# Performance work log

Measured on AMD Instinct MI355X. Metric: run time of the kernel, lower is better.

The kernel has to match this reference:

```python
import jax, jax.numpy as jnp
import numpy as np

H = 128          # rnn_hid_size
SEQ_LEN = 2048
B = 4096
IN = 2           # SELECT_SIZE * 2


def _uniform(key, shape, stdv):
    return jax.random.uniform(key, shape, jnp.float32, -stdv, stdv)


def setup_inputs() -> dict:
    key = jax.random.key(0)
    ks = jax.random.split(key, 20)
    values = jax.random.normal(ks[0], (B, SEQ_LEN, 3), jnp.float32)
    masks = (jax.random.uniform(ks[1], (B, SEQ_LEN)) > 0.5).astype(jnp.float32)
    deltas = jax.random.uniform(ks[2], (B, SEQ_LEN, 3), jnp.float32)
    eval_masks = (jax.random.uniform(ks[3], (B, SEQ_LEN)) > 0.5).astype(jnp.float32)
    s = 1.0 / np.sqrt(H)
    params = {
        'Wih0': _uniform(ks[4], (4 * H, IN), s), 'Whh0': _uniform(ks[5], (4 * H, H), s),
        'bih0': _uniform(ks[6], (4 * H,), s), 'bhh0': _uniform(ks[7], (4 * H,), s),
        'Wih1': _uniform(ks[8], (4 * H, IN), s), 'Whh1': _uniform(ks[9], (4 * H, H), s),
        'bih1': _uniform(ks[10], (4 * H,), s), 'bhh1': _uniform(ks[11], (4 * H,), s),
        'td_W': _uniform(ks[12], (H, 1), s), 'td_b': _uniform(ks[13], (H,), s),
        'hr_W': _uniform(ks[14], (1, H), 1.0 / np.sqrt(H)), 'hr_b': _uniform(ks[15], (1,), 1.0 / np.sqrt(H)),
    }
    return dict(values=values, masks=masks, deltas=deltas, eval_masks=eval_masks, **params)


def _lstm_cell(x, h, c, Wih, Whh, bih, bhh):
    g = x @ Wih.T + bih + h @ Whh.T + bhh            # [B, 4H]
    i, f, gg, o = jnp.split(g, 4, axis=1)
    c2 = jax.nn.sigmoid(f) * c + jax.nn.sigmoid(i) * jnp.tanh(gg)
    h2 = jax.nn.sigmoid(o) * jnp.tanh(c2)
    return h2, c2


def reference(values, masks, deltas, eval_masks,
              Wih0, Whh0, bih0, bhh0, Wih1, Whh1, bih1, bhh1,
              td_W, td_b, hr_W, hr_b):
    bsize = values.shape[0]
    # time-major sequences for scan
    x_seq = jnp.transpose(values[:, :, 2:3], (1, 0, 2))      # [T, B, 1]
    m_seq = jnp.transpose(masks[:, :, None], (1, 0, 2))      # [T, B, 1]
    d_seq = jnp.transpose(deltas[:, :, 2:3], (1, 0, 2))      # [T, B, 1]
    in1_seq = jnp.transpose(values[:, :, 0:2], (1, 0, 2))    # [T, B, 2]

    h0 = jnp.zeros((bsize, H), jnp.float32)
    h1 = jnp.zeros((bsize, H), jnp.float32)
    c1 = jnp.zeros((bsize, H), jnp.float32)
    loss0 = jnp.zeros((), jnp.float32)

    def step(carry, inp):
        h0, h1, c1, loss = carry
        x_y, m_y, d_y, in1 = inp
        gamma_h = jnp.exp(-jax.nn.relu(d_y @ td_W.T + td_b))  # [B, H]
        x_h = h0 @ hr_W.T + hr_b                              # [B, 1]
        x_c = m_y * x_y + (1.0 - m_y) * x_h
        loss = loss + jnp.sum(jnp.square(x_y - x_h) * m_y) / (jnp.sum(m_y) + 1e-05)
        h1n, c1n = _lstm_cell(in1, h1, c1, Wih1, Whh1, bih1, bhh1)
        h1n = h1n * gamma_h
        inputs = jnp.concatenate([x_c, m_y], axis=1)          # [B, 2]
        h0n, _ = _lstm_cell(inputs, h1n, c1n, Wih0, Whh0, bih0, bhh0)
        return (h0n, h1n, c1n, loss), x_c

    (_, _, _, loss), imp = jax.lax.scan(step, (h0, h1, c1, loss0),
                                        (x_seq, m_seq, d_seq, in1_seq))
    imputations = jnp.transpose(imp, (1, 0, 2))               # [B, T, 1]
    evals = values[:, :, 2:3]
    return (loss, imputations, eval_masks[:, :, None], evals, masks[:, :, None])
```

## Files before the change

### kernel.cpp

```cpp
#include <hip/hip_runtime.h>

typedef __attribute__((ext_vector_type(8))) short bf16x8;
typedef __attribute__((ext_vector_type(4))) float f32x4;

#define L2E 1.4426950408889634f

__device__ __forceinline__ short f2bf(float x){
  unsigned u = __builtin_bit_cast(unsigned, x);
  u += 0x7fffu + ((u >> 16) & 1u);
  return (short)(u >> 16);
}
__device__ __forceinline__ float sigm(float x){
  float e = __builtin_amdgcn_exp2f(-x * L2E);
  return __builtin_amdgcn_rcpf(1.0f + e);
}
__device__ __forceinline__ float tanh_(float x){
  float e = __builtin_amdgcn_exp2f(x * (2.0f * L2E));
  return 1.0f - 2.0f * __builtin_amdgcn_rcpf(1.0f + e);
}
__device__ __forceinline__ void bar_lds(){
  asm volatile("s_waitcnt lgkmcnt(0)\n\ts_barrier" ::: "memory");
}

__global__ __launch_bounds__(512, 2)
void rios_main(const float* __restrict__ values, const float* __restrict__ masks,
               const float* __restrict__ deltas,
               const float* __restrict__ Wih0, const float* __restrict__ Whh0,
               const float* __restrict__ bih0, const float* __restrict__ bhh0,
               const float* __restrict__ Wih1, const float* __restrict__ Whh1,
               const float* __restrict__ bih1, const float* __restrict__ bhh1,
               const float* __restrict__ td_W, const float* __restrict__ td_b,
               const float* __restrict__ hr_W, const float* __restrict__ hr_b,
               float* __restrict__ out, float* __restrict__ lossws)
{
  __shared__ short hb[2][16][136];
  __shared__ float xh_part[8][16];
  __shared__ float sA[2][5][16][16];
  __shared__ float impbuf[2][16][20];
  __shared__ float lossbuf[2][16][2];

  const int tid = threadIdx.x;
  const int w  = tid >> 6;
  const int l  = tid & 63;
  const int q  = l >> 4;
  const int c  = l & 15;
  const int q4 = q << 2;
  const int u  = (w << 4) + c;
  const long long bb = (long long)blockIdx.x * 16;

  bf16x8 wf[2][4][4];
  {
    const float* WhhA[2] = { Whh1, Whh0 };
    #pragma unroll
    for (int cell = 0; cell < 2; ++cell)
      #pragma unroll
      for (int gi = 0; gi < 4; ++gi)
        #pragma unroll
        for (int kt = 0; kt < 4; ++kt){
          const float* rp = WhhA[cell] + (((gi << 7) + u) << 7) + (kt << 5) + (q << 3);
          bf16x8 f;
          #pragma unroll
          for (int j = 0; j < 8; ++j) f[j] = f2bf(rp[j]);
          wf[cell][gi][kt] = f;
        }
  }
  float wi[2][4][2], bs[2][4];
  {
    const float* WihA[2] = { Wih1, Wih0 };
    const float* bihA[2] = { bih1, bih0 };
    const float* bhhA[2] = { bhh1, bhh0 };
    #pragma unroll
    for (int cell = 0; cell < 2; ++cell)
      #pragma unroll
      for (int gi = 0; gi < 4; ++gi){
        int rg = (gi << 7) + u;
        wi[cell][gi][0] = WihA[cell][rg * 2];
        wi[cell][gi][1] = WihA[cell][rg * 2 + 1];
        bs[cell][gi]    = bihA[cell][rg] + bhhA[cell][rg];
      }
  }
  const float tdw = td_W[u], tdbv = td_b[u], hrw = hr_W[u], hrb = hr_b[0];

  {
    short* hz = &hb[0][0][0];
    for (int i = tid; i < 16 * 136; i += 512) hz[i] = 0;
    if (tid < 128) ((float*)xh_part)[tid] = 0.f;
  }

  const int isV = (tid < 192);
  const int isD = (tid >= 192 && tid < 384);
  const int isM = (tid >= 384 && tid < 448);
  int lb = 0, lp = 0;
  if (isV){ lb = tid / 12;        lp = tid % 12; }
  else if (isD){ lb = (tid-192)/12; lp = (tid-192)%12; }
  else if (isM){ lb = (tid-384)/4;  lp = (tid-384)%4; }
  const float* ldbase = nullptr;
  if (isV)      ldbase = values + ((bb + lb) * 2048LL) * 3 + lp * 4;
  else if (isD) ldbase = deltas + ((bb + lb) * 2048LL) * 3 + lp * 4;
  else if (isM) ldbase = masks  +  (bb + lb) * 2048LL      + lp * 4;

  auto write_stage = [&](int buf, f32x4 r){
    if (isV){
      #pragma unroll
      for (int j = 0; j < 4; ++j){ int idx = lp * 4 + j; sA[buf][idx % 3][idx / 3][lb] = r[j]; }
    } else if (isD){
      #pragma unroll
      for (int j = 0; j < 4; ++j){ int idx = lp * 4 + j; if (idx % 3 == 2) sA[buf][4][idx / 3][lb] = r[j]; }
    } else if (isM){
      #pragma unroll
      for (int j = 0; j < 4; ++j){ sA[buf][3][lp * 4 + j][lb] = r[j]; }
    }
  };

  if (tid < 448){
    f32x4 st = *(const f32x4*)(ldbase);
    write_stage(0, st);
  }
  __syncthreads();

  f32x4 c1 = {0.f, 0.f, 0.f, 0.f};

  for (int cc = 0; cc < 128; ++cc){
    const int cb = cc & 1;
    f32x4 nst;
    if (cc + 1 < 128 && tid < 448){
      long long t0 = (long long)(cc + 1) * 16;
      nst = *(const f32x4*)(ldbase + (isM ? t0 : t0 * 3));
    }
    #pragma unroll 2
    for (int tt = 0; tt < 16; ++tt){
      const int t = (cc << 4) + tt;
      const int p = tt & 1;

      f32x4 v0v = *(const f32x4*)&sA[cb][0][tt][q4];
      f32x4 v1v = *(const f32x4*)&sA[cb][1][tt][q4];
      f32x4 dv  = *(const f32x4*)&sA[cb][4][tt][q4];
      f32x4 acc[4];
      #pragma unroll
      for (int gi = 0; gi < 4; ++gi){
        #pragma unroll
        for (int r = 0; r < 4; ++r)
          acc[gi][r] = fmaf(v0v[r], wi[0][gi][0], fmaf(v1v[r], wi[0][gi][1], bs[0][gi]));
      }
      #pragma unroll
      for (int kt = 0; kt < 4; ++kt){
        bf16x8 af = *(const bf16x8*)&hb[p][c][(kt << 5) + (q << 3)];
        #pragma unroll
        for (int gi = 0; gi < 4; ++gi)
          acc[gi] = __builtin_amdgcn_mfma_f32_16x16x32_bf16(af, wf[0][gi][kt], acc[gi], 0, 0, 0);
      }

      if (w == 0){
        f32x4 xh = { hrb, hrb, hrb, hrb };
        #pragma unroll
        for (int w2 = 0; w2 < 8; ++w2)
          xh += *(const f32x4*)&xh_part[w2][q4];
        f32x4 xy = *(const f32x4*)&sA[cb][2][tt][q4];
        f32x4 mm = *(const f32x4*)&sA[cb][3][tt][q4];
        f32x4 xc = mm * xy + (1.f - mm) * xh;
        f32x4 df = xy - xh;
        f32x4 wv = df * df * mm;
        if (c == 0) *((f32x4*)&impbuf[cb][tt][q4]) = xc;
        float swse = wv[0] + wv[1] + wv[2] + wv[3];
        float smm  = mm[0] + mm[1] + mm[2] + mm[3];
        swse += __shfl_xor(swse, 16); swse += __shfl_xor(swse, 32);
        smm  += __shfl_xor(smm, 16);  smm  += __shfl_xor(smm, 32);
        if (l == 0){ lossbuf[cb][tt][0] = swse; lossbuf[cb][tt][1] = smm; }
      }

      #pragma unroll
      for (int r = 0; r < 4; ++r){
        float si = sigm(acc[0][r]);
        float sf = sigm(acc[1][r]);
        float tg = tanh_(acc[2][r]);
        float so = sigm(acc[3][r]);
        float c2 = sf * c1[r] + si * tg;
        float a1 = fmaxf(fmaf(dv[r], tdw, tdbv), 0.f);
        float gam = __builtin_amdgcn_exp2f(-a1 * L2E);
        float h1n = so * tanh_(c2) * gam;
        c1[r] = c2;
        hb[p ^ 1][q4 + r][u] = f2bf(h1n);
      }
      bar_lds();

      f32x4 xcv = *(const f32x4*)&impbuf[cb][tt][q4];
      f32x4 mmv = *(const f32x4*)&sA[cb][3][tt][q4];
      #pragma unroll
      for (int gi = 0; gi < 4; ++gi){
        #pragma unroll
        for (int r = 0; r < 4; ++r)
          acc[gi][r] = fmaf(xcv[r], wi[1][gi][0], fmaf(mmv[r], wi[1][gi][1], bs[1][gi]));
      }
      #pragma unroll
      for (int kt = 0; kt < 4; ++kt){
        bf16x8 af = *(const bf16x8*)&hb[p ^ 1][c][(kt << 5) + (q << 3)];
        #pragma unroll
        for (int gi = 0; gi < 4; ++gi)
          acc[gi] = __builtin_amdgcn_mfma_f32_16x16x32_bf16(af, wf[1][gi][kt], acc[gi], 0, 0, 0);
      }
      f32x4 pv;
      #pragma unroll
      for (int r = 0; r < 4; ++r){
        float si = sigm(acc[0][r]);
        float sf = sigm(acc[1][r]);
        float tg = tanh_(acc[2][r]);
        float so = sigm(acc[3][r]);
        float c0n = sf * c1[r] + si * tg;
        float h0n = so * tanh_(c0n);
        pv[r] = h0n * hrw;
      }
      #pragma unroll
      for (int mk = 1; mk < 16; mk <<= 1){
        #pragma unroll
        for (int r = 0; r < 4; ++r) pv[r] += __shfl_xor(pv[r], mk);
      }
      if (c == 0) *((f32x4*)&xh_part[w][q4]) = pv;
      bar_lds();
    }
    if (cc + 1 < 128 && tid < 448) write_stage(cb ^ 1, nst);
    bar_lds();
    if (tid < 256){
      int m = tid >> 4, ttf = tid & 15;
      out[1 + (bb + m) * 2048LL + (cc << 4) + ttf] = impbuf[cb][ttf][m];
    } else if (tid < 288){
      int k = tid - 256;
      int ttf = k >> 1;
      atomicAdd(&lossws[(((cc << 4) + ttf) << 1) + (k & 1)], lossbuf[cb][ttf][k & 1]);
    }
  }
}

__global__ void loss_reduce(const float* __restrict__ lossws, float* __restrict__ out){
  __shared__ float red[1024];
  int t = threadIdx.x;
  float v = lossws[2 * t] / (lossws[2 * t + 1] + 1e-5f)
          + lossws[2 * (t + 1024)] / (lossws[2 * (t + 1024) + 1] + 1e-5f);
  red[t] = v;
  __syncthreads();
  for (int s = 512; s > 0; s >>= 1){
    if (t < s) red[t] += red[t + s];
    __syncthreads();
  }
  if (t == 0) out[0] = red[0];
}

__global__ void copy_outs(const float* __restrict__ values, const float* __restrict__ masks,
                          const float* __restrict__ evalm, float* __restrict__ out){
  const long long M = 8388608LL;
  long long i = (long long)blockIdx.x * 256 + threadIdx.x;
  if (i < M){
    out[1 + M     + i] = evalm[i];
    out[1 + 2 * M + i] = values[3 * i + 2];
    out[1 + 3 * M + i] = masks[i];
  }
}

extern "C" void kernel_launch(void* const* d_in, const int* in_sizes, int n_in,
                              void* d_out, int out_size, void* d_ws, size_t ws_size,
                              hipStream_t stream){
  const float* values = (const float*)d_in[0];
  const float* masks  = (const float*)d_in[1];
  const float* deltas = (const float*)d_in[2];
  const float* evalm  = (const float*)d_in[3];
  const float* Wih0   = (const float*)d_in[4];
  const float* Whh0   = (const float*)d_in[5];
  const float* bih0   = (const float*)d_in[6];
  const float* bhh0   = (const float*)d_in[7];
  const float* Wih1   = (const float*)d_in[8];
  const float* Whh1   = (const float*)d_in[9];
  const float* bih1   = (const float*)d_in[10];
  const float* bhh1   = (const float*)d_in[11];
  const float* td_W   = (const float*)d_in[12];
  const float* td_b   = (const float*)d_in[13];
  const float* hr_W   = (const float*)d_in[14];
  const float* hr_b   = (const float*)d_in[15];
  float* out    = (float*)d_out;
  float* lossws = (float*)d_ws;

  hipMemsetAsync(lossws, 0, 2048 * 2 * sizeof(float), stream);
  hipLaunchKernelGGL(copy_outs, dim3(32768), dim3(256), 0, stream, values, masks, evalm, out);
  hipLaunchKernelGGL(rios_main, dim3(256), dim3(512), 0, stream,
                     values, masks, deltas, Wih0, Whh0, bih0, bhh0,
                     Wih1, Whh1, bih1, bhh1, td_W, td_b, hr_W, hr_b, out, lossws);
  hipLaunchKernelGGL(loss_reduce, dim3(1), dim3(1024), 0, stream, lossws, out);
}
```

Measured before the change: 8.716 ms.

## Split the two LSTM cells across warp groups and pipeline them by one step

The block grows to 1024 threads: waves 0-7 compute cell 1 (h1, c1) for step s, while waves 8-15 compute cell 0 (h0, imputation, loss) for step s-1 in the same phase. This cuts the per-step critical path from two dependent cell evaluations with two barriers to one barrier. c1 is passed through a new shared buffer, imputation and loss flushing lag one chunk, and an epilogue finishes the last step. The cost is one block per CU with 1024 threads, which may change register pressure and occupancy.

```diff
diff --git a/kernel.cpp b/kernel.cpp
--- a/kernel.cpp
+++ b/kernel.cpp
@@ -22,7 +22,7 @@
   asm volatile("s_waitcnt lgkmcnt(0)\n\ts_barrier" ::: "memory");
 }
 
-__global__ __launch_bounds__(512, 2)
+__global__ __launch_bounds__(1024, 1)
 void rios_main(const float* __restrict__ values, const float* __restrict__ masks,
                const float* __restrict__ deltas,
                const float* __restrict__ Wih0, const float* __restrict__ Whh0,
@@ -34,56 +34,53 @@
                float* __restrict__ out, float* __restrict__ lossws)
 {
   __shared__ short hb[2][16][136];
+  __shared__ float cbf[2][16][132];
+  __shared__ float sA[2][5][16][16];
   __shared__ float xh_part[8][16];
-  __shared__ float sA[2][5][16][16];
   __shared__ float impbuf[2][16][20];
   __shared__ float lossbuf[2][16][2];
 
   const int tid = threadIdx.x;
-  const int w  = tid >> 6;
-  const int l  = tid & 63;
-  const int q  = l >> 4;
-  const int c  = l & 15;
-  const int q4 = q << 2;
-  const int u  = (w << 4) + c;
+  const int w   = tid >> 6;
+  const int isA = (w < 8);
+  const int wB  = w & 7;
+  const int l   = tid & 63;
+  const int q   = l >> 4;
+  const int c   = l & 15;
+  const int q4  = q << 2;
+  const int u   = (wB << 4) + c;
   const long long bb = (long long)blockIdx.x * 16;
 
-  bf16x8 wf[2][4][4];
-  {
-    const float* WhhA[2] = { Whh1, Whh0 };
+  const float* Whh = isA ? Whh1 : Whh0;
+  const float* Wih = isA ? Wih1 : Wih0;
+  const float* bih = isA ? bih1 : bih0;
+  const float* bhh = isA ? bhh1 : bhh0;
+
+  bf16x8 wf[4][4];
+  #pragma unroll
+  for (int gi = 0; gi < 4; ++gi)
     #pragma unroll
-    for (int cell = 0; cell < 2; ++cell)
+    for (int kt = 0; kt < 4; ++kt){
+      const float* rp = Whh + (((gi << 7) + u) << 7) + (kt << 5) + (q << 3);
+      bf16x8 f;
       #pragma unroll
-      for (int gi = 0; gi < 4; ++gi)
-        #pragma unroll
-        for (int kt = 0; kt < 4; ++kt){
-          const float* rp = WhhA[cell] + (((gi << 7) + u) << 7) + (kt << 5) + (q << 3);
-          bf16x8 f;
-          #pragma unroll
-          for (int j = 0; j < 8; ++j) f[j] = f2bf(rp[j]);
-          wf[cell][gi][kt] = f;
-        }
-  }
-  float wi[2][4][2], bs[2][4];
-  {
-    const float* WihA[2] = { Wih1, Wih0 };
-    const float* bihA[2] = { bih1, bih0 };
-    const float* bhhA[2] = { bhh1, bhh0 };
-    #pragma unroll
-    for (int cell = 0; cell < 2; ++cell)
-      #pragma unroll
-      for (int gi = 0; gi < 4; ++gi){
-        int rg = (gi << 7) + u;
-        wi[cell][gi][0] = WihA[cell][rg * 2];
-        wi[cell][gi][1] = WihA[cell][rg * 2 + 1];
-        bs[cell][gi]    = bihA[cell][rg] + bhhA[cell][rg];
-      }
-  }
-  const float tdw = td_W[u], tdbv = td_b[u], hrw = hr_W[u], hrb = hr_b[0];
+      for (int j = 0; j < 8; ++j) f[j] = f2bf(rp[j]);
+      wf[gi][kt] = f;
+    }
+  float wi0[4], wi1[4], bs[4];
+  #pragma unroll
+  for (int gi = 0; gi < 4; ++gi){
+    int rg = (gi << 7) + u;
+    wi0[gi] = Wih[rg * 2];
+    wi1[gi] = Wih[rg * 2 + 1];
+    bs[gi]  = bih[rg] + bhh[rg];
+  }
+  const float tdw = td_W[u], tdbv = td_b[u];
+  const float hrw = hr_W[u], hrb = hr_b[0];
 
   {
     short* hz = &hb[0][0][0];
-    for (int i = tid; i < 16 * 136; i += 512) hz[i] = 0;
+    for (int i = tid; i < 16 * 136; i += 1024) hz[i] = 0;
     if (tid < 128) ((float*)xh_part)[tid] = 0.f;
   }
 
@@ -129,104 +126,136 @@
     }
     #pragma unroll 2
     for (int tt = 0; tt < 16; ++tt){
-      const int t = (cc << 4) + tt;
-      const int p = tt & 1;
-
-      f32x4 v0v = *(const f32x4*)&sA[cb][0][tt][q4];
-      f32x4 v1v = *(const f32x4*)&sA[cb][1][tt][q4];
-      f32x4 dv  = *(const f32x4*)&sA[cb][4][tt][q4];
-      f32x4 acc[4];
-      #pragma unroll
-      for (int gi = 0; gi < 4; ++gi){
-        #pragma unroll
-        for (int r = 0; r < 4; ++r)
-          acc[gi][r] = fmaf(v0v[r], wi[0][gi][0], fmaf(v1v[r], wi[0][gi][1], bs[0][gi]));
-      }
-      #pragma unroll
-      for (int kt = 0; kt < 4; ++kt){
-        bf16x8 af = *(const bf16x8*)&hb[p][c][(kt << 5) + (q << 3)];
-        #pragma unroll
-        for (int gi = 0; gi < 4; ++gi)
-          acc[gi] = __builtin_amdgcn_mfma_f32_16x16x32_bf16(af, wf[0][gi][kt], acc[gi], 0, 0, 0);
-      }
-
-      if (w == 0){
+      const int s  = (cc << 4) + tt;
+      const int pr = s & 1;
+
+      if (isA){
+        if (s < 2047){
+          f32x4 v0v = *(const f32x4*)&sA[cb][0][tt][q4];
+          f32x4 v1v = *(const f32x4*)&sA[cb][1][tt][q4];
+          f32x4 dv  = *(const f32x4*)&sA[cb][4][tt][q4];
+          f32x4 acc[4];
+          #pragma unroll
+          for (int gi = 0; gi < 4; ++gi){
+            #pragma unroll
+            for (int r = 0; r < 4; ++r)
+              acc[gi][r] = fmaf(v0v[r], wi0[gi], fmaf(v1v[r], wi1[gi], bs[gi]));
+          }
+          #pragma unroll
+          for (int kt = 0; kt < 4; ++kt){
+            bf16x8 af = *(const bf16x8*)&hb[pr][c][(kt << 5) + (q << 3)];
+            #pragma unroll
+            for (int gi = 0; gi < 4; ++gi)
+              acc[gi] = __builtin_amdgcn_mfma_f32_16x16x32_bf16(af, wf[gi][kt], acc[gi], 0, 0, 0);
+          }
+          #pragma unroll
+          for (int r = 0; r < 4; ++r){
+            float si = sigm(acc[0][r]);
+            float sf = sigm(acc[1][r]);
+            float tg = tanh_(acc[2][r]);
+            float so = sigm(acc[3][r]);
+            float c2 = sf * c1[r] + si * tg;
+            float a1 = fmaxf(fmaf(dv[r], tdw, tdbv), 0.f);
+            float gam = __builtin_amdgcn_exp2f(-a1 * L2E);
+            float h1n = so * tanh_(c2) * gam;
+            c1[r] = c2;
+            cbf[pr ^ 1][q4 + r][u] = c2;
+            hb[pr ^ 1][q4 + r][u]  = f2bf(h1n);
+          }
+        }
+      } else if (s > 0){
+        const int tb  = s - 1;
+        const int cbB = (tb >> 4) & 1;
+        const int ttb = tb & 15;
         f32x4 xh = { hrb, hrb, hrb, hrb };
         #pragma unroll
         for (int w2 = 0; w2 < 8; ++w2)
           xh += *(const f32x4*)&xh_part[w2][q4];
-        f32x4 xy = *(const f32x4*)&sA[cb][2][tt][q4];
-        f32x4 mm = *(const f32x4*)&sA[cb][3][tt][q4];
+        f32x4 xy = *(const f32x4*)&sA[cbB][2][ttb][q4];
+        f32x4 mm = *(const f32x4*)&sA[cbB][3][ttb][q4];
         f32x4 xc = mm * xy + (1.f - mm) * xh;
-        f32x4 df = xy - xh;
-        f32x4 wv = df * df * mm;
-        if (c == 0) *((f32x4*)&impbuf[cb][tt][q4]) = xc;
-        float swse = wv[0] + wv[1] + wv[2] + wv[3];
-        float smm  = mm[0] + mm[1] + mm[2] + mm[3];
-        swse += __shfl_xor(swse, 16); swse += __shfl_xor(swse, 32);
-        smm  += __shfl_xor(smm, 16);  smm  += __shfl_xor(smm, 32);
-        if (l == 0){ lossbuf[cb][tt][0] = swse; lossbuf[cb][tt][1] = smm; }
-      }
-
-      #pragma unroll
-      for (int r = 0; r < 4; ++r){
-        float si = sigm(acc[0][r]);
-        float sf = sigm(acc[1][r]);
-        float tg = tanh_(acc[2][r]);
-        float so = sigm(acc[3][r]);
-        float c2 = sf * c1[r] + si * tg;
-        float a1 = fmaxf(fmaf(dv[r], tdw, tdbv), 0.f);
-        float gam = __builtin_amdgcn_exp2f(-a1 * L2E);
-        float h1n = so * tanh_(c2) * gam;
-        c1[r] = c2;
-        hb[p ^ 1][q4 + r][u] = f2bf(h1n);
+        if (wB == 0){
+          f32x4 df = xy - xh;
+          f32x4 wv = df * df * mm;
+          if (c == 0) *((f32x4*)&impbuf[cbB][ttb][q4]) = xc;
+          float swse = wv[0] + wv[1] + wv[2] + wv[3];
+          float smm  = mm[0] + mm[1] + mm[2] + mm[3];
+          swse += __shfl_xor(swse, 16); swse += __shfl_xor(swse, 32);
+          smm  += __shfl_xor(smm, 16);  smm  += __shfl_xor(smm, 32);
+          if (l == 0){ lossbuf[cbB][ttb][0] = swse; lossbuf[cbB][ttb][1] = smm; }
+        }
+        f32x4 acc[4];
+        #pragma unroll
+        for (int gi = 0; gi < 4; ++gi){
+          #pragma unroll
+          for (int r = 0; r < 4; ++r)
+            acc[gi][r] = fmaf(xc[r], wi0[gi], fmaf(mm[r], wi1[gi], bs[gi]));
+        }
+        #pragma unroll
+        for (int kt = 0; kt < 4; ++kt){
+          bf16x8 af = *(const bf16x8*)&hb[pr][c][(kt << 5) + (q << 3)];
+          #pragma unroll
+          for (int gi = 0; gi < 4; ++gi)
+            acc[gi] = __builtin_amdgcn_mfma_f32_16x16x32_bf16(af, wf[gi][kt], acc[gi], 0, 0, 0);
+        }
+        f32x4 pv;
+        #pragma unroll
+        for (int r = 0; r < 4; ++r){
+          float c1v = cbf[pr][q4 + r][u];
+          float si = sigm(acc[0][r]);
+          float sf = sigm(acc[1][r]);
+          float tg = tanh_(acc[2][r]);
+          float so = sigm(acc[3][r]);
+          float c0n = sf * c1v + si * tg;
+          float h0n = so * tanh_(c0n);
+          pv[r] = h0n * hrw;
+        }
+        #pragma unroll
+        for (int mk = 1; mk < 16; mk <<= 1){
+          #pragma unroll
+          for (int r = 0; r < 4; ++r) pv[r] += __shfl_xor(pv[r], mk);
+        }
+        if (c == 0) *((f32x4*)&xh_part[wB][q4]) = pv;
       }
       bar_lds();
-
-      f32x4 xcv = *(const f32x4*)&impbuf[cb][tt][q4];
-      f32x4 mmv = *(const f32x4*)&sA[cb][3][tt][q4];
-      #pragma unroll
-      for (int gi = 0; gi < 4; ++gi){
-        #pragma unroll
-        for (int r = 0; r < 4; ++r)
-          acc[gi][r] = fmaf(xcv[r], wi[1][gi][0], fmaf(mmv[r], wi[1][gi][1], bs[1][gi]));
+    }
+    if (cc + 1 < 128 && tid < 448) write_stage(cb ^ 1, nst);
+    if (cc >= 1){
+      if (tid < 256){
+        int m = tid >> 4, ttf = tid & 15;
+        out[1 + (bb + m) * 2048LL + ((cc - 1) << 4) + ttf] = impbuf[cb ^ 1][ttf][m];
+      } else if (tid < 288){
+        int k = tid - 256, ttf = k >> 1;
+        atomicAdd(&lossws[((((cc - 1) << 4) + ttf) << 1) + (k & 1)], lossbuf[cb ^ 1][ttf][k & 1]);
       }
-      #pragma unroll
-      for (int kt = 0; kt < 4; ++kt){
-        bf16x8 af = *(const bf16x8*)&hb[p ^ 1][c][(kt << 5) + (q << 3)];
-        #pragma unroll
-        for (int gi = 0; gi < 4; ++gi)
-          acc[gi] = __builtin_amdgcn_mfma_f32_16x16x32_bf16(af, wf[1][gi][kt], acc[gi], 0, 0, 0);
-      }
-      f32x4 pv;
-      #pragma unroll
-      for (int r = 0; r < 4; ++r){
-        float si = sigm(acc[0][r]);
-        float sf = sigm(acc[1][r]);
-        float tg = tanh_(acc[2][r]);
-        float so = sigm(acc[3][r]);
-        float c0n = sf * c1[r] + si * tg;
-        float h0n = so * tanh_(c0n);
-        pv[r] = h0n * hrw;
-      }
-      #pragma unroll
-      for (int mk = 1; mk < 16; mk <<= 1){
-        #pragma unroll
-        for (int r = 0; r < 4; ++r) pv[r] += __shfl_xor(pv[r], mk);
-      }
-      if (c == 0) *((f32x4*)&xh_part[w][q4]) = pv;
-      bar_lds();
-    }
-    if (cc + 1 < 128 && tid < 448) write_stage(cb ^ 1, nst);
+    }
     bar_lds();
-    if (tid < 256){
-      int m = tid >> 4, ttf = tid & 15;
-      out[1 + (bb + m) * 2048LL + (cc << 4) + ttf] = impbuf[cb][ttf][m];
-    } else if (tid < 288){
-      int k = tid - 256;
-      int ttf = k >> 1;
-      atomicAdd(&lossws[(((cc << 4) + ttf) << 1) + (k & 1)], lossbuf[cb][ttf][k & 1]);
-    }
+  }
+
+  if (w == 8){
+    f32x4 xh = { hrb, hrb, hrb, hrb };
+    #pragma unroll
+    for (int w2 = 0; w2 < 8; ++w2)
+      xh += *(const f32x4*)&xh_part[w2][q4];
+    f32x4 xy = *(const f32x4*)&sA[1][2][15][q4];
+    f32x4 mm = *(const f32x4*)&sA[1][3][15][q4];
+    f32x4 xc = mm * xy + (1.f - mm) * xh;
+    f32x4 df = xy - xh;
+    f32x4 wv = df * df * mm;
+    if (c == 0) *((f32x4*)&impbuf[1][15][q4]) = xc;
+    float swse = wv[0] + wv[1] + wv[2] + wv[3];
+    float smm  = mm[0] + mm[1] + mm[2] + mm[3];
+    swse += __shfl_xor(swse, 16); swse += __shfl_xor(swse, 32);
+    smm  += __shfl_xor(smm, 16);  smm  += __shfl_xor(smm, 32);
+    if (l == 0){ lossbuf[1][15][0] = swse; lossbuf[1][15][1] = smm; }
+  }
+  bar_lds();
+  if (tid < 256){
+    int m = tid >> 4, ttf = tid & 15;
+    out[1 + (bb + m) * 2048LL + 2032 + ttf] = impbuf[1][ttf][m];
+  } else if (tid < 288){
+    int k = tid - 256, ttf = k >> 1;
+    atomicAdd(&lossws[((2032 + ttf) << 1) + (k & 1)], lossbuf[1][ttf][k & 1]);
   }
 }
 
@@ -279,7 +308,7 @@
 
   hipMemsetAsync(lossws, 0, 2048 * 2 * sizeof(float), stream);
   hipLaunchKernelGGL(copy_outs, dim3(32768), dim3(256), 0, stream, values, masks, evalm, out);
-  hipLaunchKernelGGL(rios_main, dim3(256), dim3(512), 0, stream,
+  hipLaunchKernelGGL(rios_main, dim3(256), dim3(1024), 0, stream,
                      values, masks, deltas, Wih0, Whh0, bih0, bhh0,
                      Wih1, Whh1, bih1, bhh1, td_W, td_b, hr_W, hr_b, out, lossws);
   hipLaunchKernelGGL(loss_reduce, dim3(1), dim3(1024), 0, stream, lossws, out);
```

Result: slower. 14.80 ms (+69.8%).
